# Performance work log

Measured on AMD Instinct MI355X. Metric: run time of the kernel, lower is better.

## Reference

```python
import jax, jax.numpy as jnp
from jax import lax
import numpy as np

B, H, W, C = 8, 64, 64, 128   # NHWC input
F = 256                        # output filters
KH = KW = 3
K = KH * KW
DG = 1                         # deformable groups
CG = C // DG                   # channels per deformable group
PAD_Y, PAD_X = (KH - 1) // 2, (KW - 1) // 2  # SAME padding, stride 1, dilation 1


def setup_inputs() -> dict:
    k1, k2, k3 = jax.random.split(jax.random.key(0), 3)
    return {
        "inputs": jax.random.normal(k1, (B, H, W, C), jnp.float32),
        # conv_offset: Conv2D(dg*3*kh*kw, kernel_size, padding='same', use_bias=True)
        "offset_kernel": jax.random.normal(k2, (KH, KW, C, DG * 3 * K), jnp.float32) * 0.01,
        "offset_bias": jnp.zeros((DG * 3 * K,), jnp.float32),
        # main filter, HWIO as built for channels_last
        "filt": jax.random.normal(k3, (KH, KW, C, F), jnp.float32) * 0.05,
    }


def _deform_conv2d(inputs, offset_kernel, offset_bias, filt):
    # 1) predict offsets + modulation mask with a plain conv (stride 1, SAME)
    wi = lax.conv_general_dilated(
        inputs, offset_kernel, (1, 1), "SAME",
        dimension_numbers=("NHWC", "HWIO", "NHWC")) + offset_bias
    o1, o2, m = jnp.split(wi, 3, axis=-1)           # each [B,H,W,DG*K]
    mask = jax.nn.sigmoid(m).reshape(B, H, W, DG, K)

    # 2) sampling coordinates: base conv grid + learned offsets (o1 = y, o2 = x)
    ky, kx = jnp.meshgrid(jnp.arange(KH), jnp.arange(KW), indexing="ij")
    base_y = (jnp.arange(H)[:, None] - PAD_Y + ky.reshape(-1)[None, :]).astype(jnp.float32)  # [H,K]
    base_x = (jnp.arange(W)[:, None] - PAD_X + kx.reshape(-1)[None, :]).astype(jnp.float32)  # [W,K]
    py = base_y[None, :, None, None, :] + o1.reshape(B, H, W, DG, K)  # [B,H,W,DG,K]
    px = base_x[None, None, :, None, :] + o2.reshape(B, H, W, DG, K)

    # 3) modulated bilinear sampling with zero padding outside the image
    img = inputs.reshape(B, H, W, DG, CG)
    y0f = jnp.floor(py)
    x0f = jnp.floor(px)
    wy1 = py - y0f
    wy0 = 1.0 - wy1
    wx1 = px - x0f
    wx0 = 1.0 - wx1
    bidx = jnp.arange(B)[:, None, None, None, None]
    gidx = jnp.arange(DG)[None, None, None, :, None]

    def corner(yf, xf, wgt):
        valid = (yf >= 0) & (yf <= H - 1) & (xf >= 0) & (xf <= W - 1)
        yi = jnp.clip(yf, 0, H - 1).astype(jnp.int32)
        xi = jnp.clip(xf, 0, W - 1).astype(jnp.int32)
        v = img[bidx, yi, xi, gidx]                  # [B,H,W,DG,K,CG]
        return v * (wgt * valid.astype(jnp.float32))[..., None]

    sampled = (corner(y0f, x0f, wy0 * wx0)
               + corner(y0f, x0f + 1.0, wy0 * wx1)
               + corner(y0f + 1.0, x0f, wy1 * wx0)
               + corner(y0f + 1.0, x0f + 1.0, wy1 * wx1))
    sampled = sampled * mask[..., None]              # DCNv2 modulation

    # 4) im2col columns -> GEMM with the main filter (num_groups = 1)
    cols = jnp.moveaxis(sampled, 3, 4).reshape(B, H, W, K, C)  # channels dg-major
    return jnp.einsum("bhwkc,kcf->bhwf", cols, filt.reshape(K, C, F))


def reference(inputs, offset_kernel, offset_bias, filt):
    return _deform_conv2d(inputs, offset_kernel, offset_bias, filt)
```

## Files before the change

kernel.cpp:

```cpp
#include <hip/hip_runtime.h>
#include <hip/hip_fp16.h>
#include <math.h>

#define B_  8
#define H_  64
#define W_  64
#define C_  128
#define F_  256
#define NOC 27

typedef float    f32x4 __attribute__((ext_vector_type(4)));
typedef _Float16 f16x8 __attribute__((ext_vector_type(8)));

#define FILTT_OFF_F 32768
#define WI32_OFF_F  180224
#define INH_OFF_F   1228800
#define AIM_OFF_F   3325952

static __device__ __forceinline__ unsigned pkh2(float a, float b) {
    __half2 h = __floats2half2_rn(a, b);
    union { __half2 h2; unsigned u; } cv; cv.h2 = h;
    return cv.u;
}

static __device__ __forceinline__ void async16(void* lds, const void* g) {
    __builtin_amdgcn_global_load_lds(
        (const __attribute__((address_space(1))) unsigned int*)g,
        (__attribute__((address_space(3))) unsigned int*)lds, 16, 0, 0);
}

__global__ __launch_bounds__(256) void prep(const float* __restrict__ kofs,
                                            const float* __restrict__ filt,
                                            const float* __restrict__ in,
                                            unsigned short* __restrict__ woffT,
                                            unsigned short* __restrict__ filtT2,
                                            unsigned short* __restrict__ inh) {
    int bidx = blockIdx.x;
    if (bidx >= 1296) {
        int gid = (bidx - 1296) * 256 + threadIdx.x;
        const float4* ip = reinterpret_cast<const float4*>(in) + (size_t)gid * 4;
        float4 a = ip[0], b = ip[1], c = ip[2], d = ip[3];
        uint4 r0 = make_uint4(pkh2(a.x, a.y), pkh2(a.z, a.w), pkh2(b.x, b.y), pkh2(b.z, b.w));
        uint4 r1 = make_uint4(pkh2(c.x, c.y), pkh2(c.z, c.w), pkh2(d.x, d.y), pkh2(d.z, d.w));
        uint4* op = reinterpret_cast<uint4*>(inh) + (size_t)gid * 2;
        op[0] = r0; op[1] = r1;
        return;
    }
    int idx = bidx * 256 + threadIdx.x;
    if (idx < 9 * 32 * 128) {
        int tap = idx >> 12;
        int r   = idx & 4095;
        int oc  = r >> 7;
        int c   = r & 127;
        float v = (oc < NOC) ? kofs[(tap * C_ + c) * NOC + oc] : 0.f;
        union { __half h; unsigned short u; } cv; cv.h = __float2half(v);
        woffT[idx] = cv.u;
        return;
    }
    int idx2 = idx - 9 * 32 * 128;
    if (idx2 < 9 * 256 * 128) {
        int tap = idx2 / 32768;
        int r   = idx2 & 32767;
        int f   = r >> 7;
        int c   = r & 127;
        float v = filt[(tap * C_ + c) * F_ + f];
        union { __half h; unsigned short u; } cv; cv.h = __float2half(v);
        filtT2[(size_t)f * 1152 + tap * 128 + c] = cv.u;
    }
}

__global__ __launch_bounds__(256) void offset_conv_mfma(const unsigned short* __restrict__ inh,
                                                        const unsigned short* __restrict__ woffT,
                                                        const float* __restrict__ bias,
                                                        float* __restrict__ wi32) {
    __shared__ __align__(16) unsigned char win[3 * 66 * 256];

    int t    = threadIdx.x;
    int bid  = blockIdx.x;
    int lg   = ((bid & 7) << 6) | (bid >> 3);
    int bb   = lg >> 6;
    int hh   = lg & 63;
    int pix0 = lg << 6;

    for (int idx = t; idx < 3 * 66 * 16; idx += 256) {
        int ky = idx / (66 * 16);
        int r  = idx % (66 * 16);
        int xi = r >> 4;
        int c8 = r & 15;
        int y  = hh + ky - 1;
        int x  = xi - 1;
        uint4 v = make_uint4(0u, 0u, 0u, 0u);
        if ((unsigned)y < 64u && (unsigned)x < 64u)
            v = *(const uint4*)((const char*)inh +
                    ((size_t)(((bb << 6) + y) * 64 + x) << 8) + (c8 << 4));
        *(uint4*)(win + ky * 16896 + xi * 256 + ((c8 << 4) ^ ((xi & 7) << 4))) = v;
    }
    __syncthreads();

    int lane = t & 63, wv = t >> 6;
    int row  = lane & 15, kg = lane >> 4;
    int px0  = wv << 4;

    f32x4 z = {0.f, 0.f, 0.f, 0.f};
    f32x4 acc[2] = {z, z};

    for (int tap = 0; tap < 9; ++tap) {
        int ky = tap / 3, kx = tap - ky * 3;
        int xi = px0 + row + kx;
        const unsigned char* arow = win + ky * 16896 + xi * 256;
        int sw = (xi & 7) << 4;
        const unsigned short* bp = woffT + (size_t)tap * 4096 + (size_t)row * 128 + kg * 8;
        #pragma unroll
        for (int ks = 0; ks < 4; ++ks) {
            f16x8 a  = *(const f16x8*)(arow + ((ks * 64 + kg * 16) ^ sw));
            f16x8 b0 = *(const f16x8*)(bp + ks * 32);
            f16x8 b1 = *(const f16x8*)(bp + 2048 + ks * 32);
            acc[0] = __builtin_amdgcn_mfma_f32_16x16x32_f16(a, b0, acc[0], 0, 0, 0);
            acc[1] = __builtin_amdgcn_mfma_f32_16x16x32_f16(a, b1, acc[1], 0, 0, 0);
        }
    }

    #pragma unroll
    for (int n = 0; n < 2; ++n) {
        int oc = n * 16 + row;
        float bv = (oc < NOC) ? bias[oc] : 0.f;
        #pragma unroll
        for (int r = 0; r < 4; ++r) {
            int px = px0 + kg * 4 + r;
            wi32[(size_t)(pix0 + px) * 32 + oc] = acc[n][r] + bv;
        }
    }
}

__global__ __launch_bounds__(256) void sample_a(const unsigned short* __restrict__ inh,
                                                const float* __restrict__ wi32,
                                                unsigned short* __restrict__ Aim) {
    __shared__ __align__(16) uint4 offs[8][9];
    __shared__ __align__(16) uint2 wgts[8][9];

    int t   = threadIdx.x;
    int bid = blockIdx.x;
    int lg  = ((bid & 7) << 9) | (bid >> 3);
    int pix0 = lg << 3;

    if (t < 72) {
        int pxl = t / 9, tap = t - pxl * 9;
        int pix = pix0 + pxl;
        int bb  = pix >> 12;
        int hh  = (pix >> 6) & 63;
        int col = pix & 63;
        const float* wp = wi32 + (size_t)pix * 32;
        float o1 = wp[tap], o2 = wp[9 + tap], mm = wp[18 + tap];
        float mask = 1.f / (1.f + __expf(-mm));
        int ky = tap / 3, kx = tap - ky * 3;
        float py  = (float)(hh - 1 + ky) + o1;
        float pxx = (float)(col - 1 + kx) + o2;
        float y0f = floorf(py), x0f = floorf(pxx);
        float wy1 = py - y0f,  wy0 = 1.f - wy1;
        float wx1 = pxx - x0f, wx0 = 1.f - wx1;
        float vy0 = (y0f >=  0.f && y0f <= 63.f) ? 1.f : 0.f;
        float vy1 = (y0f >= -1.f && y0f <= 62.f) ? 1.f : 0.f;
        float vx0 = (x0f >=  0.f && x0f <= 63.f) ? 1.f : 0.f;
        float vx1 = (x0f >= -1.f && x0f <= 62.f) ? 1.f : 0.f;
        int y0 = (int)fminf(fmaxf(y0f,       0.f), 63.f);
        int y1 = (int)fminf(fmaxf(y0f + 1.f, 0.f), 63.f);
        int x0 = (int)fminf(fmaxf(x0f,       0.f), 63.f);
        int x1 = (int)fminf(fmaxf(x0f + 1.f, 0.f), 63.f);
        int base = bb << 12;
        offs[pxl][tap] = make_uint4((unsigned)((base + (y0 << 6) + x0) << 8),
                                    (unsigned)((base + (y0 << 6) + x1) << 8),
                                    (unsigned)((base + (y1 << 6) + x0) << 8),
                                    (unsigned)((base + (y1 << 6) + x1) << 8));
        wgts[pxl][tap] = make_uint2(pkh2(wy0 * wx0 * mask * vy0 * vx0,
                                         wy0 * wx1 * mask * vy0 * vx1),
                                    pkh2(wy1 * wx0 * mask * vy1 * vx0,
                                         wy1 * wx1 * mask * vy1 * vx1));
    }
    __syncthreads();

    int c8  = t & 15;
    int pxl = (t >> 4) & 7;
    int th  = t >> 7;
    int cb  = c8 << 4;

    const char* ih = (const char*)inh;
    char* Ao = (char*)Aim + (size_t)(pix0 + pxl) * 2304;

    int tbeg = th ? 5 : 0, tend = th ? 9 : 5;
    union AU { uint4 u; __half2 h[4]; };
    #pragma unroll 5
    for (int tap = tbeg; tap < tend; ++tap) {
        uint4 O  = offs[pxl][tap];
        uint2 Wp = wgts[pxl][tap];
        union { unsigned u; __half2 h; } w00, w01, w10, w11;
        w00.u = (Wp.x & 0xFFFFu) * 0x10001u;
        w01.u = (Wp.x >> 16)     * 0x10001u;
        w10.u = (Wp.y & 0xFFFFu) * 0x10001u;
        w11.u = (Wp.y >> 16)     * 0x10001u;
        AU c00, c01, c10, c11, s;
        c00.u = *(const uint4*)(ih + O.x + cb);
        c01.u = *(const uint4*)(ih + O.y + cb);
        c10.u = *(const uint4*)(ih + O.z + cb);
        c11.u = *(const uint4*)(ih + O.w + cb);
        #pragma unroll
        for (int j = 0; j < 4; ++j) {
            __half2 sj = __hmul2(c00.h[j], w00.h);
            sj = __hfma2(c01.h[j], w01.h, sj);
            sj = __hfma2(c10.h[j], w10.h, sj);
            s.h[j] = __hfma2(c11.h[j], w11.h, sj);
        }
        *(uint4*)(Ao + tap * 256 + cb) = s.u;
    }
}

__global__ __launch_bounds__(256) void gemm_im2col(const unsigned short* __restrict__ Aim,
                                                   const unsigned short* __restrict__ filtT2,
                                                   float* __restrict__ out) {
    __shared__ __align__(16) unsigned char As[16384];
    __shared__ __align__(16) unsigned char Bs[16384];

    int t   = threadIdx.x;
    int bid = blockIdx.x;
    int lg  = ((bid & 7) << 6) | (bid >> 3);
    int mt  = lg >> 1, nt = lg & 1;
    int apix = mt << 7;
    int f0   = nt << 7;

    int lane = t & 63, wv = t >> 6;
    int wm = wv & 1, wn = wv >> 1;
    int row16 = lane & 15, kg = lane >> 4;

    const char* Ab = (const char*)Aim;
    const char* Bb = (const char*)filtT2;

    f32x4 z = {0.f, 0.f, 0.f, 0.f};
    f32x4 acc[4][4];
    #pragma unroll
    for (int m = 0; m < 4; ++m)
        #pragma unroll
        for (int n = 0; n < 4; ++n) acc[m][n] = z;

    int lin0 = wv * 1024 + lane * 16;

    for (int kb = 0; kb < 18; ++kb) {
        int k2 = kb << 7;
        #pragma unroll
        for (int it = 0; it < 4; ++it) {
            int lin  = lin0 + it * 4096;
            int arow = lin >> 7;
            int acol = (lin & 127) ^ ((arow & 7) << 4);
            async16(As + wv * 1024 + it * 4096,
                    Ab + (size_t)(apix + arow) * 2304 + k2 + acol);
            async16(Bs + wv * 1024 + it * 4096,
                    Bb + (size_t)(f0 + arow) * 2304 + k2 + acol);
        }
        __syncthreads();

        int sw = (row16 & 7) << 4;
        #pragma unroll
        for (int ks = 0; ks < 2; ++ks) {
            int kcol = ((ks << 6) + (kg << 4)) ^ sw;
            f16x8 a[4], b[4];
            #pragma unroll
            for (int m = 0; m < 4; ++m)
                a[m] = *(const f16x8*)(As + ((wm << 6) + (m << 4) + row16) * 128 + kcol);
            #pragma unroll
            for (int n = 0; n < 4; ++n)
                b[n] = *(const f16x8*)(Bs + ((wn << 6) + (n << 4) + row16) * 128 + kcol);
            #pragma unroll
            for (int m = 0; m < 4; ++m)
                #pragma unroll
                for (int n = 0; n < 4; ++n)
                    acc[m][n] = __builtin_amdgcn_mfma_f32_16x16x32_f16(a[m], b[n], acc[m][n], 0, 0, 0);
        }
        __syncthreads();
    }

    int pxb = apix + (wm << 6);
    int fcb = f0 + (wn << 6) + row16;
    #pragma unroll
    for (int m = 0; m < 4; ++m)
        #pragma unroll
        for (int r = 0; r < 4; ++r) {
            int px = pxb + (m << 4) + (kg << 2) + r;
            float* op = out + (size_t)px * 256 + fcb;
            op[0]  = acc[m][0][r];
            op[16] = acc[m][1][r];
            op[32] = acc[m][2][r];
            op[48] = acc[m][3][r];
        }
}

extern "C" void kernel_launch(void* const* d_in, const int* in_sizes, int n_in,
                              void* d_out, int out_size, void* d_ws, size_t ws_size,
                              hipStream_t stream) {
    const float* in   = (const float*)d_in[0];
    const float* kofs = (const float*)d_in[1];
    const float* bias = (const float*)d_in[2];
    const float* filt = (const float*)d_in[3];
    float* out = (float*)d_out;
    float* ws  = (float*)d_ws;

    unsigned short* woffT  = (unsigned short*)ws;
    unsigned short* filtT2 = (unsigned short*)(ws + FILTT_OFF_F);
    float*          wi32   = ws + WI32_OFF_F;
    unsigned short* inh    = (unsigned short*)(ws + INH_OFF_F);
    unsigned short* Aim    = (unsigned short*)(ws + AIM_OFF_F);

    hipLaunchKernelGGL(prep, dim3(2320), dim3(256), 0, stream, kofs, filt, in, woffT, filtT2, inh);
    hipLaunchKernelGGL(offset_conv_mfma, dim3(512), dim3(256), 0, stream, inh, woffT, bias, wi32);
    hipLaunchKernelGGL(sample_a, dim3(4096), dim3(256), 0, stream, inh, wi32, Aim);
    hipLaunchKernelGGL(gemm_im2col, dim3(512), dim3(256), 0, stream, Aim, filtT2, out);
}
```

Baseline: 76.78 us.

## Fuse bilinear sampling into im2col GEMM with double-buffered LDS pipeline

Removes the separate sample_a kernel and the materialized fp16 im2col buffer. The GEMM kernel now computes the bilinear sampling parameters per pixel and tap, gathers the four corners and blends them directly into swizzled LDS A tiles. Two ping-pong A/B buffers overlap the next tap's gathers and async filter loads with the current MFMA work. This saves one launch and the Aim write and read, but the sampling work is repeated for each of the two N tiles and register pressure rises.

```diff
diff --git a/kernel.cpp b/kernel.cpp
--- a/kernel.cpp
+++ b/kernel.cpp
@@ -15,7 +15,6 @@
 #define FILTT_OFF_F 32768
 #define WI32_OFF_F  180224
 #define INH_OFF_F   1228800
-#define AIM_OFF_F   3325952
 
 static __device__ __forceinline__ unsigned pkh2(float a, float b) {
     __half2 h = __floats2half2_rn(a, b);
@@ -132,92 +131,101 @@
     }
 }
 
-__global__ __launch_bounds__(256) void sample_a(const unsigned short* __restrict__ inh,
-                                                const float* __restrict__ wi32,
-                                                unsigned short* __restrict__ Aim) {
-    __shared__ __align__(16) uint4 offs[8][9];
-    __shared__ __align__(16) uint2 wgts[8][9];
-
-    int t   = threadIdx.x;
-    int bid = blockIdx.x;
-    int lg  = ((bid & 7) << 9) | (bid >> 3);
-    int pix0 = lg << 3;
-
-    if (t < 72) {
-        int pxl = t / 9, tap = t - pxl * 9;
-        int pix = pix0 + pxl;
-        int bb  = pix >> 12;
-        int hh  = (pix >> 6) & 63;
-        int col = pix & 63;
-        const float* wp = wi32 + (size_t)pix * 32;
-        float o1 = wp[tap], o2 = wp[9 + tap], mm = wp[18 + tap];
-        float mask = 1.f / (1.f + __expf(-mm));
-        int ky = tap / 3, kx = tap - ky * 3;
-        float py  = (float)(hh - 1 + ky) + o1;
-        float pxx = (float)(col - 1 + kx) + o2;
-        float y0f = floorf(py), x0f = floorf(pxx);
-        float wy1 = py - y0f,  wy0 = 1.f - wy1;
-        float wx1 = pxx - x0f, wx0 = 1.f - wx1;
-        float vy0 = (y0f >=  0.f && y0f <= 63.f) ? 1.f : 0.f;
-        float vy1 = (y0f >= -1.f && y0f <= 62.f) ? 1.f : 0.f;
-        float vx0 = (x0f >=  0.f && x0f <= 63.f) ? 1.f : 0.f;
-        float vx1 = (x0f >= -1.f && x0f <= 62.f) ? 1.f : 0.f;
-        int y0 = (int)fminf(fmaxf(y0f,       0.f), 63.f);
-        int y1 = (int)fminf(fmaxf(y0f + 1.f, 0.f), 63.f);
-        int x0 = (int)fminf(fmaxf(x0f,       0.f), 63.f);
-        int x1 = (int)fminf(fmaxf(x0f + 1.f, 0.f), 63.f);
-        int base = bb << 12;
-        offs[pxl][tap] = make_uint4((unsigned)((base + (y0 << 6) + x0) << 8),
-                                    (unsigned)((base + (y0 << 6) + x1) << 8),
-                                    (unsigned)((base + (y1 << 6) + x0) << 8),
-                                    (unsigned)((base + (y1 << 6) + x1) << 8));
-        wgts[pxl][tap] = make_uint2(pkh2(wy0 * wx0 * mask * vy0 * vx0,
-                                         wy0 * wx1 * mask * vy0 * vx1),
-                                    pkh2(wy1 * wx0 * mask * vy1 * vx0,
-                                         wy1 * wx1 * mask * vy1 * vx1));
-    }
-    __syncthreads();
-
-    int c8  = t & 15;
-    int pxl = (t >> 4) & 7;
-    int th  = t >> 7;
-    int cb  = c8 << 4;
-
-    const char* ih = (const char*)inh;
-    char* Ao = (char*)Aim + (size_t)(pix0 + pxl) * 2304;
-
-    int tbeg = th ? 5 : 0, tend = th ? 9 : 5;
-    union AU { uint4 u; __half2 h[4]; };
-    #pragma unroll 5
-    for (int tap = tbeg; tap < tend; ++tap) {
-        uint4 O  = offs[pxl][tap];
-        uint2 Wp = wgts[pxl][tap];
-        union { unsigned u; __half2 h; } w00, w01, w10, w11;
-        w00.u = (Wp.x & 0xFFFFu) * 0x10001u;
-        w01.u = (Wp.x >> 16)     * 0x10001u;
-        w10.u = (Wp.y & 0xFFFFu) * 0x10001u;
-        w11.u = (Wp.y >> 16)     * 0x10001u;
-        AU c00, c01, c10, c11, s;
-        c00.u = *(const uint4*)(ih + O.x + cb);
-        c01.u = *(const uint4*)(ih + O.y + cb);
-        c10.u = *(const uint4*)(ih + O.z + cb);
-        c11.u = *(const uint4*)(ih + O.w + cb);
-        #pragma unroll
-        for (int j = 0; j < 4; ++j) {
-            __half2 sj = __hmul2(c00.h[j], w00.h);
-            sj = __hfma2(c01.h[j], w01.h, sj);
-            sj = __hfma2(c10.h[j], w10.h, sj);
-            s.h[j] = __hfma2(c11.h[j], w11.h, sj);
-        }
-        *(uint4*)(Ao + tap * 256 + cb) = s.u;
-    }
-}
-
-__global__ __launch_bounds__(256) void gemm_im2col(const unsigned short* __restrict__ Aim,
-                                                   const unsigned short* __restrict__ filtT2,
-                                                   float* __restrict__ out) {
-    __shared__ __align__(16) unsigned char As[16384];
-    __shared__ __align__(16) unsigned char Bs[16384];
+struct Par { unsigned o00, o01, o10, o11, wa, wb; };
+
+static __device__ __forceinline__ Par mkpar(float o1, float o2, float mm,
+                                            int hh, int col, int bb, int tap) {
+    float mask = 1.f / (1.f + __expf(-mm));
+    int ky = tap / 3, kx = tap - ky * 3;
+    float py  = (float)(hh - 1 + ky) + o1;
+    float pxx = (float)(col - 1 + kx) + o2;
+    float y0f = floorf(py), x0f = floorf(pxx);
+    float wy1 = py - y0f,  wy0 = 1.f - wy1;
+    float wx1 = pxx - x0f, wx0 = 1.f - wx1;
+    float vy0 = (y0f >=  0.f && y0f <= 63.f) ? 1.f : 0.f;
+    float vy1 = (y0f >= -1.f && y0f <= 62.f) ? 1.f : 0.f;
+    float vx0 = (x0f >=  0.f && x0f <= 63.f) ? 1.f : 0.f;
+    float vx1 = (x0f >= -1.f && x0f <= 62.f) ? 1.f : 0.f;
+    int y0 = (int)fminf(fmaxf(y0f,       0.f), 63.f);
+    int y1 = (int)fminf(fmaxf(y0f + 1.f, 0.f), 63.f);
+    int x0 = (int)fminf(fmaxf(x0f,       0.f), 63.f);
+    int x1 = (int)fminf(fmaxf(x0f + 1.f, 0.f), 63.f);
+    int base = bb << 12;
+    Par p;
+    p.o00 = (unsigned)((base + (y0 << 6) + x0) << 8);
+    p.o01 = (unsigned)((base + (y0 << 6) + x1) << 8);
+    p.o10 = (unsigned)((base + (y1 << 6) + x0) << 8);
+    p.o11 = (unsigned)((base + (y1 << 6) + x1) << 8);
+    p.wa  = pkh2(wy0 * wx0 * mask * vy0 * vx0, wy0 * wx1 * mask * vy0 * vx1);
+    p.wb  = pkh2(wy1 * wx0 * mask * vy1 * vx0, wy1 * wx1 * mask * vy1 * vx1);
+    return p;
+}
+
+static __device__ __forceinline__ void issue_corners(uint4 cc[4][4], const char* ih,
+                                                     const Par& p, int chb) {
+    #pragma unroll
+    for (int j = 0; j < 4; ++j) cc[0][j] = *(const uint4*)(ih + p.o00 + chb + j * 16);
+    #pragma unroll
+    for (int j = 0; j < 4; ++j) cc[1][j] = *(const uint4*)(ih + p.o01 + chb + j * 16);
+    #pragma unroll
+    for (int j = 0; j < 4; ++j) cc[2][j] = *(const uint4*)(ih + p.o10 + chb + j * 16);
+    #pragma unroll
+    for (int j = 0; j < 4; ++j) cc[3][j] = *(const uint4*)(ih + p.o11 + chb + j * 16);
+}
+
+static __device__ __forceinline__ void blend_write(unsigned char* dst, int spx, int cp,
+                                                   const uint4 cc[4][4],
+                                                   unsigned wa, unsigned wb) {
+    union H2 { unsigned u; __half2 h; };
+    H2 w00, w01, w10, w11;
+    w00.u = (wa & 0xFFFFu) * 0x10001u;
+    w01.u = (wa >> 16)     * 0x10001u;
+    w10.u = (wb & 0xFFFFu) * 0x10001u;
+    w11.u = (wb >> 16)     * 0x10001u;
+    #pragma unroll
+    for (int j = 0; j < 4; ++j) {
+        union { uint4 u; __half2 h[4]; } a0, a1, a2, a3, s;
+        a0.u = cc[0][j]; a1.u = cc[1][j]; a2.u = cc[2][j]; a3.u = cc[3][j];
+        #pragma unroll
+        for (int q = 0; q < 4; ++q) {
+            __half2 v = __hmul2(a0.h[q], w00.h);
+            v = __hfma2(a1.h[q], w01.h, v);
+            v = __hfma2(a2.h[q], w10.h, v);
+            s.h[q] = __hfma2(a3.h[q], w11.h, v);
+        }
+        int c8 = cp * 4 + j;
+        *(uint4*)(dst + spx * 128 + ((c8 * 16) ^ ((spx & 7) << 4))) = s.u;
+    }
+}
+
+static __device__ __forceinline__ void do_mfma(const unsigned char* As, const unsigned char* Bs,
+                                               int wm, int wn, int row16, int kg,
+                                               f32x4 acc[4][4]) {
+    int sw = (row16 & 7) << 4;
+    #pragma unroll
+    for (int ks = 0; ks < 2; ++ks) {
+        int kcol = ((ks << 6) + (kg << 4)) ^ sw;
+        f16x8 a[4], b[4];
+        #pragma unroll
+        for (int m = 0; m < 4; ++m)
+            a[m] = *(const f16x8*)(As + ((wm << 6) + (m << 4) + row16) * 128 + kcol);
+        #pragma unroll
+        for (int n = 0; n < 4; ++n)
+            b[n] = *(const f16x8*)(Bs + ((wn << 6) + (n << 4) + row16) * 128 + kcol);
+        #pragma unroll
+        for (int m = 0; m < 4; ++m)
+            #pragma unroll
+            for (int n = 0; n < 4; ++n)
+                acc[m][n] = __builtin_amdgcn_mfma_f32_16x16x32_f16(a[m], b[n], acc[m][n], 0, 0, 0);
+    }
+}
+
+__global__ __launch_bounds__(256, 2) void gemm_fused(const unsigned short* __restrict__ inh,
+                                                     const unsigned short* __restrict__ filtT2,
+                                                     const float* __restrict__ wi32,
+                                                     float* __restrict__ out) {
+    __shared__ __align__(16) unsigned char As0[16384], As1[16384];
+    __shared__ __align__(16) unsigned char Bs0[16384], Bs1[16384];
 
     int t   = threadIdx.x;
     int bid = blockIdx.x;
@@ -226,13 +234,20 @@
     int apix = mt << 7;
     int f0   = nt << 7;
 
+    int spx = t & 127;
+    int cp  = t >> 7;
+    int pix = apix + spx;
+    int bb  = pix >> 12, hh = (pix >> 6) & 63, col = pix & 63;
+    const float* wrow = wi32 + (size_t)pix * 32;
+    const char*  ih   = (const char*)inh;
+
     int lane = t & 63, wv = t >> 6;
+    int lin0 = wv * 1024 + lane * 16;
+    const char* Bb = (const char*)filtT2;
+
     int wm = wv & 1, wn = wv >> 1;
     int row16 = lane & 15, kg = lane >> 4;
 
-    const char* Ab = (const char*)Aim;
-    const char* Bb = (const char*)filtT2;
-
     f32x4 z = {0.f, 0.f, 0.f, 0.f};
     f32x4 acc[4][4];
     #pragma unroll
@@ -240,39 +255,50 @@
         #pragma unroll
         for (int n = 0; n < 4; ++n) acc[m][n] = z;
 
-    int lin0 = wv * 1024 + lane * 16;
-
-    for (int kb = 0; kb < 18; ++kb) {
-        int k2 = kb << 7;
+    uint4 cc[4][4];
+    Par par;
+    float no1, no2, nmm;
+
+    auto asyncB = [&](unsigned char* buf, int s) {
         #pragma unroll
         for (int it = 0; it < 4; ++it) {
             int lin  = lin0 + it * 4096;
-            int arow = lin >> 7;
-            int acol = (lin & 127) ^ ((arow & 7) << 4);
-            async16(As + wv * 1024 + it * 4096,
-                    Ab + (size_t)(apix + arow) * 2304 + k2 + acol);
-            async16(Bs + wv * 1024 + it * 4096,
-                    Bb + (size_t)(f0 + arow) * 2304 + k2 + acol);
-        }
+            int brow = lin >> 7;
+            int bcol = (lin & 127) ^ ((brow & 7) << 4);
+            async16(buf + wv * 1024 + it * 4096,
+                    Bb + (size_t)(f0 + brow) * 2304 + s * 128 + bcol);
+        }
+    };
+
+    {
+        float o1 = wrow[0], o2 = wrow[9], mm = wrow[18];
+        par = mkpar(o1, o2, mm, hh, col, bb, 0);
+        issue_corners(cc, ih, par, cp * 64);
+        asyncB(Bs0, 0);
+        no1 = wrow[1]; no2 = wrow[10]; nmm = wrow[19];
+        blend_write(As0, spx, cp, cc, par.wa, par.wb);
         __syncthreads();
-
-        int sw = (row16 & 7) << 4;
-        #pragma unroll
-        for (int ks = 0; ks < 2; ++ks) {
-            int kcol = ((ks << 6) + (kg << 4)) ^ sw;
-            f16x8 a[4], b[4];
-            #pragma unroll
-            for (int m = 0; m < 4; ++m)
-                a[m] = *(const f16x8*)(As + ((wm << 6) + (m << 4) + row16) * 128 + kcol);
-            #pragma unroll
-            for (int n = 0; n < 4; ++n)
-                b[n] = *(const f16x8*)(Bs + ((wn << 6) + (n << 4) + row16) * 128 + kcol);
-            #pragma unroll
-            for (int m = 0; m < 4; ++m)
-                #pragma unroll
-                for (int n = 0; n < 4; ++n)
-                    acc[m][n] = __builtin_amdgcn_mfma_f32_16x16x32_f16(a[m], b[n], acc[m][n], 0, 0, 0);
-        }
+    }
+
+    for (int tap = 0; tap < 9; ++tap) {
+        issue_corners(cc, ih, par, 128 + cp * 64);
+        asyncB(Bs1, 2 * tap + 1);
+        __builtin_amdgcn_sched_barrier(0);
+        do_mfma(As0, Bs0, wm, wn, row16, kg, acc);
+        blend_write(As1, spx, cp, cc, par.wa, par.wb);
+        __syncthreads();
+
+        if (tap < 8) {
+            par = mkpar(no1, no2, nmm, hh, col, bb, tap + 1);
+            if (tap < 7) {
+                no1 = wrow[tap + 2]; no2 = wrow[11 + tap]; nmm = wrow[20 + tap];
+            }
+            issue_corners(cc, ih, par, cp * 64);
+            asyncB(Bs0, 2 * tap + 2);
+            __builtin_amdgcn_sched_barrier(0);
+        }
+        do_mfma(As1, Bs1, wm, wn, row16, kg, acc);
+        if (tap < 8) blend_write(As0, spx, cp, cc, par.wa, par.wb);
         __syncthreads();
     }
 
@@ -305,10 +331,8 @@
     unsigned short* filtT2 = (unsigned short*)(ws + FILTT_OFF_F);
     float*          wi32   = ws + WI32_OFF_F;
     unsigned short* inh    = (unsigned short*)(ws + INH_OFF_F);
-    unsigned short* Aim    = (unsigned short*)(ws + AIM_OFF_F);
 
     hipLaunchKernelGGL(prep, dim3(2320), dim3(256), 0, stream, kofs, filt, in, woffT, filtT2, inh);
     hipLaunchKernelGGL(offset_conv_mfma, dim3(512), dim3(256), 0, stream, inh, woffT, bias, wi32);
-    hipLaunchKernelGGL(sample_a, dim3(4096), dim3(256), 0, stream, inh, wi32, Aim);
-    hipLaunchKernelGGL(gemm_im2col, dim3(512), dim3(256), 0, stream, Aim, filtT2, out);
-}
+    hipLaunchKernelGGL(gemm_fused, dim3(512), dim3(256), 0, stream, inh, filtT2, wi32, out);
+}
```

Measured after the change: 114.3 us. 1.49x slower.

## Fuse offset conv with bilinear sampling and double-buffer GEMM LDS stages

Applied to the files above, without the earlier changes.

Merges the offset-prediction conv and the bilinear sampling kernel into one per-row kernel, so offsets and mask stay in shared memory and are never written to or reread from a global buffer. This also removes one kernel launch. Separately, the im2col GEMM now double-buffers its A/B LDS tiles so the async loads for the next K-step are issued before the MFMAs on the current one. The fused kernel runs only 512 blocks, where the old sampling kernel used 4096, and both kernels use more LDS, which can lower occupancy and hurt latency hiding in the gather loop.

```diff
diff --git a/kernel.cpp b/kernel.cpp
--- a/kernel.cpp
+++ b/kernel.cpp
@@ -13,7 +13,6 @@
 typedef _Float16 f16x8 __attribute__((ext_vector_type(8)));
 
 #define FILTT_OFF_F 32768
-#define WI32_OFF_F  180224
 #define INH_OFF_F   1228800
 #define AIM_OFF_F   3325952
 
@@ -69,11 +68,14 @@
     }
 }
 
-__global__ __launch_bounds__(256) void offset_conv_mfma(const unsigned short* __restrict__ inh,
-                                                        const unsigned short* __restrict__ woffT,
-                                                        const float* __restrict__ bias,
-                                                        float* __restrict__ wi32) {
+__global__ __launch_bounds__(256) void sample_row(const unsigned short* __restrict__ inh,
+                                                  const unsigned short* __restrict__ woffT,
+                                                  const float* __restrict__ bias,
+                                                  unsigned short* __restrict__ Aim) {
     __shared__ __align__(16) unsigned char win[3 * 66 * 256];
+    __shared__ float wi[64][33];
+    __shared__ __align__(16) uint4 prmo[64][9];
+    __shared__ __align__(16) uint2 prmw[64][9];
 
     int t    = threadIdx.x;
     int bid  = blockIdx.x;
@@ -97,64 +99,48 @@
     }
     __syncthreads();
 
-    int lane = t & 63, wv = t >> 6;
-    int row  = lane & 15, kg = lane >> 4;
-    int px0  = wv << 4;
-
-    f32x4 z = {0.f, 0.f, 0.f, 0.f};
-    f32x4 acc[2] = {z, z};
-
-    for (int tap = 0; tap < 9; ++tap) {
-        int ky = tap / 3, kx = tap - ky * 3;
-        int xi = px0 + row + kx;
-        const unsigned char* arow = win + ky * 16896 + xi * 256;
-        int sw = (xi & 7) << 4;
-        const unsigned short* bp = woffT + (size_t)tap * 4096 + (size_t)row * 128 + kg * 8;
-        #pragma unroll
-        for (int ks = 0; ks < 4; ++ks) {
-            f16x8 a  = *(const f16x8*)(arow + ((ks * 64 + kg * 16) ^ sw));
-            f16x8 b0 = *(const f16x8*)(bp + ks * 32);
-            f16x8 b1 = *(const f16x8*)(bp + 2048 + ks * 32);
-            acc[0] = __builtin_amdgcn_mfma_f32_16x16x32_f16(a, b0, acc[0], 0, 0, 0);
-            acc[1] = __builtin_amdgcn_mfma_f32_16x16x32_f16(a, b1, acc[1], 0, 0, 0);
-        }
-    }
-
-    #pragma unroll
-    for (int n = 0; n < 2; ++n) {
-        int oc = n * 16 + row;
-        float bv = (oc < NOC) ? bias[oc] : 0.f;
-        #pragma unroll
-        for (int r = 0; r < 4; ++r) {
-            int px = px0 + kg * 4 + r;
-            wi32[(size_t)(pix0 + px) * 32 + oc] = acc[n][r] + bv;
-        }
-    }
-}
-
-__global__ __launch_bounds__(256) void sample_a(const unsigned short* __restrict__ inh,
-                                                const float* __restrict__ wi32,
-                                                unsigned short* __restrict__ Aim) {
-    __shared__ __align__(16) uint4 offs[8][9];
-    __shared__ __align__(16) uint2 wgts[8][9];
-
-    int t   = threadIdx.x;
-    int bid = blockIdx.x;
-    int lg  = ((bid & 7) << 9) | (bid >> 3);
-    int pix0 = lg << 3;
-
-    if (t < 72) {
-        int pxl = t / 9, tap = t - pxl * 9;
-        int pix = pix0 + pxl;
-        int bb  = pix >> 12;
-        int hh  = (pix >> 6) & 63;
-        int col = pix & 63;
-        const float* wp = wi32 + (size_t)pix * 32;
-        float o1 = wp[tap], o2 = wp[9 + tap], mm = wp[18 + tap];
+    {
+        int lane = t & 63, wv = t >> 6;
+        int row  = lane & 15, kg = lane >> 4;
+        int px0  = wv << 4;
+
+        f32x4 z = {0.f, 0.f, 0.f, 0.f};
+        f32x4 acc[2] = {z, z};
+
+        for (int tap = 0; tap < 9; ++tap) {
+            int ky = tap / 3, kx = tap - ky * 3;
+            int xi = px0 + row + kx;
+            const unsigned char* arow = win + ky * 16896 + xi * 256;
+            int sw = (xi & 7) << 4;
+            const unsigned short* bp = woffT + (size_t)tap * 4096 + (size_t)row * 128 + kg * 8;
+            #pragma unroll
+            for (int ks = 0; ks < 4; ++ks) {
+                f16x8 a  = *(const f16x8*)(arow + ((ks * 64 + kg * 16) ^ sw));
+                f16x8 b0 = *(const f16x8*)(bp + ks * 32);
+                f16x8 b1 = *(const f16x8*)(bp + 2048 + ks * 32);
+                acc[0] = __builtin_amdgcn_mfma_f32_16x16x32_f16(a, b0, acc[0], 0, 0, 0);
+                acc[1] = __builtin_amdgcn_mfma_f32_16x16x32_f16(a, b1, acc[1], 0, 0, 0);
+            }
+        }
+        #pragma unroll
+        for (int n = 0; n < 2; ++n) {
+            int oc = n * 16 + row;
+            float bv = (oc < NOC) ? bias[oc] : 0.f;
+            #pragma unroll
+            for (int r = 0; r < 4; ++r)
+                wi[px0 + kg * 4 + r][oc] = acc[n][r] + bv;
+        }
+    }
+    __syncthreads();
+
+    for (int it = t; it < 576; it += 256) {
+        int px  = it & 63;
+        int tap = it >> 6;
+        float o1 = wi[px][tap], o2 = wi[px][9 + tap], mm = wi[px][18 + tap];
         float mask = 1.f / (1.f + __expf(-mm));
         int ky = tap / 3, kx = tap - ky * 3;
         float py  = (float)(hh - 1 + ky) + o1;
-        float pxx = (float)(col - 1 + kx) + o2;
+        float pxx = (float)(px - 1 + kx) + o2;
         float y0f = floorf(py), x0f = floorf(pxx);
         float wy1 = py - y0f,  wy0 = 1.f - wy1;
         float wx1 = pxx - x0f, wx0 = 1.f - wx1;
@@ -167,57 +153,61 @@
         int x0 = (int)fminf(fmaxf(x0f,       0.f), 63.f);
         int x1 = (int)fminf(fmaxf(x0f + 1.f, 0.f), 63.f);
         int base = bb << 12;
-        offs[pxl][tap] = make_uint4((unsigned)((base + (y0 << 6) + x0) << 8),
-                                    (unsigned)((base + (y0 << 6) + x1) << 8),
-                                    (unsigned)((base + (y1 << 6) + x0) << 8),
-                                    (unsigned)((base + (y1 << 6) + x1) << 8));
-        wgts[pxl][tap] = make_uint2(pkh2(wy0 * wx0 * mask * vy0 * vx0,
-                                         wy0 * wx1 * mask * vy0 * vx1),
-                                    pkh2(wy1 * wx0 * mask * vy1 * vx0,
-                                         wy1 * wx1 * mask * vy1 * vx1));
+        prmo[px][tap] = make_uint4((unsigned)((base + (y0 << 6) + x0) << 8),
+                                   (unsigned)((base + (y0 << 6) + x1) << 8),
+                                   (unsigned)((base + (y1 << 6) + x0) << 8),
+                                   (unsigned)((base + (y1 << 6) + x1) << 8));
+        prmw[px][tap] = make_uint2(pkh2(wy0 * wx0 * mask * vy0 * vx0,
+                                        wy0 * wx1 * mask * vy0 * vx1),
+                                   pkh2(wy1 * wx0 * mask * vy1 * vx0,
+                                        wy1 * wx1 * mask * vy1 * vx1));
     }
     __syncthreads();
 
     int c8  = t & 15;
-    int pxl = (t >> 4) & 7;
+    int pxg = (t >> 4) & 7;
     int th  = t >> 7;
     int cb  = c8 << 4;
 
     const char* ih = (const char*)inh;
-    char* Ao = (char*)Aim + (size_t)(pix0 + pxl) * 2304;
-
     int tbeg = th ? 5 : 0, tend = th ? 9 : 5;
     union AU { uint4 u; __half2 h[4]; };
-    #pragma unroll 5
-    for (int tap = tbeg; tap < tend; ++tap) {
-        uint4 O  = offs[pxl][tap];
-        uint2 Wp = wgts[pxl][tap];
-        union { unsigned u; __half2 h; } w00, w01, w10, w11;
-        w00.u = (Wp.x & 0xFFFFu) * 0x10001u;
-        w01.u = (Wp.x >> 16)     * 0x10001u;
-        w10.u = (Wp.y & 0xFFFFu) * 0x10001u;
-        w11.u = (Wp.y >> 16)     * 0x10001u;
-        AU c00, c01, c10, c11, s;
-        c00.u = *(const uint4*)(ih + O.x + cb);
-        c01.u = *(const uint4*)(ih + O.y + cb);
-        c10.u = *(const uint4*)(ih + O.z + cb);
-        c11.u = *(const uint4*)(ih + O.w + cb);
-        #pragma unroll
-        for (int j = 0; j < 4; ++j) {
-            __half2 sj = __hmul2(c00.h[j], w00.h);
-            sj = __hfma2(c01.h[j], w01.h, sj);
-            sj = __hfma2(c10.h[j], w10.h, sj);
-            s.h[j] = __hfma2(c11.h[j], w11.h, sj);
-        }
-        *(uint4*)(Ao + tap * 256 + cb) = s.u;
+
+    #pragma unroll 2
+    for (int pp = 0; pp < 8; ++pp) {
+        int px = pxg + (pp << 3);
+        char* Ao = (char*)Aim + (size_t)(pix0 + px) * 2304;
+        #pragma unroll 5
+        for (int tap = tbeg; tap < tend; ++tap) {
+            uint4 O  = prmo[px][tap];
+            uint2 Wp = prmw[px][tap];
+            union { unsigned u; __half2 h; } w00, w01, w10, w11;
+            w00.u = (Wp.x & 0xFFFFu) * 0x10001u;
+            w01.u = (Wp.x >> 16)     * 0x10001u;
+            w10.u = (Wp.y & 0xFFFFu) * 0x10001u;
+            w11.u = (Wp.y >> 16)     * 0x10001u;
+            AU c00, c01, c10, c11, s;
+            c00.u = *(const uint4*)(ih + O.x + cb);
+            c01.u = *(const uint4*)(ih + O.y + cb);
+            c10.u = *(const uint4*)(ih + O.z + cb);
+            c11.u = *(const uint4*)(ih + O.w + cb);
+            #pragma unroll
+            for (int j = 0; j < 4; ++j) {
+                __half2 sj = __hmul2(c00.h[j], w00.h);
+                sj = __hfma2(c01.h[j], w01.h, sj);
+                sj = __hfma2(c10.h[j], w10.h, sj);
+                s.h[j] = __hfma2(c11.h[j], w11.h, sj);
+            }
+            *(uint4*)(Ao + tap * 256 + cb) = s.u;
+        }
     }
 }
 
 __global__ __launch_bounds__(256) void gemm_im2col(const unsigned short* __restrict__ Aim,
                                                    const unsigned short* __restrict__ filtT2,
                                                    float* __restrict__ out) {
-    __shared__ __align__(16) unsigned char As[16384];
-    __shared__ __align__(16) unsigned char Bs[16384];
+    __shared__ __align__(16) unsigned char As[2][16384];
+    __shared__ __align__(16) unsigned char Bs[2][16384];
 
     int t   = threadIdx.x;
     int bid = blockIdx.x;
@@ -242,20 +232,21 @@
 
     int lin0 = wv * 1024 + lane * 16;
 
-    for (int kb = 0; kb < 18; ++kb) {
-        int k2 = kb << 7;
+    auto stageTo = [&](unsigned char* A, unsigned char* B, int s) {
+        int k2 = s << 7;
         #pragma unroll
         for (int it = 0; it < 4; ++it) {
-            int lin  = lin0 + it * 4096;
-            int arow = lin >> 7;
-            int acol = (lin & 127) ^ ((arow & 7) << 4);
-            async16(As + wv * 1024 + it * 4096,
-                    Ab + (size_t)(apix + arow) * 2304 + k2 + acol);
-            async16(Bs + wv * 1024 + it * 4096,
-                    Bb + (size_t)(f0 + arow) * 2304 + k2 + acol);
-        }
-        __syncthreads();
-
+            int lin = lin0 + it * 4096;
+            int r_  = lin >> 7;
+            int c_  = (lin & 127) ^ ((r_ & 7) << 4);
+            async16(A + wv * 1024 + it * 4096,
+                    Ab + (size_t)(apix + r_) * 2304 + k2 + c_);
+            async16(B + wv * 1024 + it * 4096,
+                    Bb + (size_t)(f0 + r_) * 2304 + k2 + c_);
+        }
+    };
+
+    auto mfmaOn = [&](const unsigned char* A, const unsigned char* B) {
         int sw = (row16 & 7) << 4;
         #pragma unroll
         for (int ks = 0; ks < 2; ++ks) {
@@ -263,16 +254,28 @@
             f16x8 a[4], b[4];
             #pragma unroll
             for (int m = 0; m < 4; ++m)
-                a[m] = *(const f16x8*)(As + ((wm << 6) + (m << 4) + row16) * 128 + kcol);
+                a[m] = *(const f16x8*)(A + ((wm << 6) + (m << 4) + row16) * 128 + kcol);
             #pragma unroll
             for (int n = 0; n < 4; ++n)
-                b[n] = *(const f16x8*)(Bs + ((wn << 6) + (n << 4) + row16) * 128 + kcol);
+                b[n] = *(const f16x8*)(B + ((wn << 6) + (n << 4) + row16) * 128 + kcol);
             #pragma unroll
             for (int m = 0; m < 4; ++m)
                 #pragma unroll
                 for (int n = 0; n < 4; ++n)
                     acc[m][n] = __builtin_amdgcn_mfma_f32_16x16x32_f16(a[m], b[n], acc[m][n], 0, 0, 0);
         }
+    };
+
+    stageTo(As[0], Bs[0], 0);
+    __syncthreads();
+
+    #pragma unroll 1
+    for (int kb = 0; kb < 18; kb += 2) {
+        stageTo(As[1], Bs[1], kb + 1);
+        mfmaOn(As[0], Bs[0]);
+        __syncthreads();
+        if (kb < 16) stageTo(As[0], Bs[0], kb + 2);
+        mfmaOn(As[1], Bs[1]);
         __syncthreads();
     }
 
@@ -303,12 +306,10 @@
 
     unsigned short* woffT  = (unsigned short*)ws;
     unsigned short* filtT2 = (unsigned short*)(ws + FILTT_OFF_F);
-    float*          wi32   = ws + WI32_OFF_F;
     unsigned short* inh    = (unsigned short*)(ws + INH_OFF_F);
     unsigned short* Aim    = (unsigned short*)(ws + AIM_OFF_F);
 
     hipLaunchKernelGGL(prep, dim3(2320), dim3(256), 0, stream, kofs, filt, in, woffT, filtT2, inh);
-    hipLaunchKernelGGL(offset_conv_mfma, dim3(512), dim3(256), 0, stream, inh, woffT, bias, wi32);
-    hipLaunchKernelGGL(sample_a, dim3(4096), dim3(256), 0, stream, inh, wi32, Aim);
+    hipLaunchKernelGGL(sample_row, dim3(512), dim3(256), 0, stream, inh, woffT, bias, Aim);
     hipLaunchKernelGGL(gemm_im2col, dim3(512), dim3(256), 0, stream, Aim, filtT2, out);
 }
```

After: 73.41 us, median of 2. -4.4%, faster.

## Fuse bilinear sampling and im2col GEMM with producer/consumer warp specialization

Applied to the files above, without the earlier changes.

Merges the sampling kernel and the im2col GEMM into one kernel, so the fp16 im2col matrix is no longer written to and re-read from global memory. Within each 512-thread block, four waves gather and modulate the samples for one tap into a double-buffered LDS ring. The other four waves run MFMA on that tap, reading filter fragments directly from global memory and raising their priority with s_setprio. Each block now covers a 64-pixel row across all 256 filters. In exchange, filter loads are no longer staged through LDS, and the gather and compute stages are serialized by a block barrier on every tap.

```diff
diff --git a/kernel.cpp b/kernel.cpp
--- a/kernel.cpp
+++ b/kernel.cpp
@@ -15,18 +15,11 @@
 #define FILTT_OFF_F 32768
 #define WI32_OFF_F  180224
 #define INH_OFF_F   1228800
-#define AIM_OFF_F   3325952
 
 static __device__ __forceinline__ unsigned pkh2(float a, float b) {
     __half2 h = __floats2half2_rn(a, b);
     union { __half2 h2; unsigned u; } cv; cv.h2 = h;
     return cv.u;
-}
-
-static __device__ __forceinline__ void async16(void* lds, const void* g) {
-    __builtin_amdgcn_global_load_lds(
-        (const __attribute__((address_space(1))) unsigned int*)g,
-        (__attribute__((address_space(3))) unsigned int*)lds, 16, 0, 0);
 }
 
 __global__ __launch_bounds__(256) void prep(const float* __restrict__ kofs,
@@ -132,29 +125,33 @@
     }
 }
 
-__global__ __launch_bounds__(256) void sample_a(const unsigned short* __restrict__ inh,
-                                                const float* __restrict__ wi32,
-                                                unsigned short* __restrict__ Aim) {
-    __shared__ __align__(16) uint4 offs[8][9];
-    __shared__ __align__(16) uint2 wgts[8][9];
-
-    int t   = threadIdx.x;
-    int bid = blockIdx.x;
-    int lg  = ((bid & 7) << 9) | (bid >> 3);
-    int pix0 = lg << 3;
-
-    if (t < 72) {
-        int pxl = t / 9, tap = t - pxl * 9;
-        int pix = pix0 + pxl;
-        int bb  = pix >> 12;
-        int hh  = (pix >> 6) & 63;
-        int col = pix & 63;
-        const float* wp = wi32 + (size_t)pix * 32;
+__global__ __launch_bounds__(512, 4) void dcn_fused(const unsigned short* __restrict__ inh,
+                                                    const unsigned short* __restrict__ filtT2,
+                                                    const float* __restrict__ wi32,
+                                                    float* __restrict__ out) {
+    __shared__ __align__(16) unsigned char ring[2][64 * 256];
+    __shared__ __align__(16) uint4 prmo[64][9];
+    __shared__ __align__(16) uint2 prmw[64][9];
+
+    int t    = threadIdx.x;
+    int bid  = blockIdx.x;
+    int lg   = ((bid & 7) << 6) | (bid >> 3);
+    int bb   = lg >> 6;
+    int hh   = lg & 63;
+    int pix0 = lg << 6;
+
+    const char* ih = (const char*)inh;
+    const char* Bb = (const char*)filtT2;
+
+    for (int it = t; it < 576; it += 512) {
+        int px  = it & 63;
+        int tap = it >> 6;
+        const float* wp = wi32 + (size_t)(pix0 + px) * 32;
         float o1 = wp[tap], o2 = wp[9 + tap], mm = wp[18 + tap];
         float mask = 1.f / (1.f + __expf(-mm));
         int ky = tap / 3, kx = tap - ky * 3;
         float py  = (float)(hh - 1 + ky) + o1;
-        float pxx = (float)(col - 1 + kx) + o2;
+        float pxx = (float)(px - 1 + kx) + o2;
         float y0f = floorf(py), x0f = floorf(pxx);
         float wy1 = py - y0f,  wy0 = 1.f - wy1;
         float wx1 = pxx - x0f, wx0 = 1.f - wx1;
@@ -167,128 +164,108 @@
         int x0 = (int)fminf(fmaxf(x0f,       0.f), 63.f);
         int x1 = (int)fminf(fmaxf(x0f + 1.f, 0.f), 63.f);
         int base = bb << 12;
-        offs[pxl][tap] = make_uint4((unsigned)((base + (y0 << 6) + x0) << 8),
-                                    (unsigned)((base + (y0 << 6) + x1) << 8),
-                                    (unsigned)((base + (y1 << 6) + x0) << 8),
-                                    (unsigned)((base + (y1 << 6) + x1) << 8));
-        wgts[pxl][tap] = make_uint2(pkh2(wy0 * wx0 * mask * vy0 * vx0,
-                                         wy0 * wx1 * mask * vy0 * vx1),
-                                    pkh2(wy1 * wx0 * mask * vy1 * vx0,
-                                         wy1 * wx1 * mask * vy1 * vx1));
+        prmo[px][tap] = make_uint4((unsigned)((base + (y0 << 6) + x0) << 8),
+                                   (unsigned)((base + (y0 << 6) + x1) << 8),
+                                   (unsigned)((base + (y1 << 6) + x0) << 8),
+                                   (unsigned)((base + (y1 << 6) + x1) << 8));
+        prmw[px][tap] = make_uint2(pkh2(wy0 * wx0 * mask * vy0 * vx0,
+                                        wy0 * wx1 * mask * vy0 * vx1),
+                                   pkh2(wy1 * wx0 * mask * vy1 * vx0,
+                                        wy1 * wx1 * mask * vy1 * vx1));
     }
     __syncthreads();
 
-    int c8  = t & 15;
-    int pxl = (t >> 4) & 7;
-    int th  = t >> 7;
-    int cb  = c8 << 4;
-
-    const char* ih = (const char*)inh;
-    char* Ao = (char*)Aim + (size_t)(pix0 + pxl) * 2304;
-
-    int tbeg = th ? 5 : 0, tend = th ? 9 : 5;
+    int lane  = t & 63;
+    int wv    = t >> 6;
+    bool cons = (wv < 4);
+    int row16 = lane & 15, kg = lane >> 4;
+    const char* fb = Bb + (size_t)((wv << 6) + row16) * 2304 + (kg << 4);
+    int sw = (row16 & 7) << 4;
+    int pl = t & 255;
+    int ppx = pl >> 2;
+    int pq  = pl & 3;
+
+    f32x4 z = {0.f, 0.f, 0.f, 0.f};
+    f32x4 acc[4][4];
+    #pragma unroll
+    for (int m = 0; m < 4; ++m)
+        #pragma unroll
+        for (int n = 0; n < 4; ++n) acc[m][n] = z;
+
     union AU { uint4 u; __half2 h[4]; };
-    #pragma unroll 5
-    for (int tap = tbeg; tap < tend; ++tap) {
-        uint4 O  = offs[pxl][tap];
-        uint2 Wp = wgts[pxl][tap];
+
+    auto gather = [&](int tap, int slot) {
+        uint4 O  = prmo[ppx][tap];
+        uint2 Wp = prmw[ppx][tap];
         union { unsigned u; __half2 h; } w00, w01, w10, w11;
         w00.u = (Wp.x & 0xFFFFu) * 0x10001u;
         w01.u = (Wp.x >> 16)     * 0x10001u;
         w10.u = (Wp.y & 0xFFFFu) * 0x10001u;
         w11.u = (Wp.y >> 16)     * 0x10001u;
-        AU c00, c01, c10, c11, s;
-        c00.u = *(const uint4*)(ih + O.x + cb);
-        c01.u = *(const uint4*)(ih + O.y + cb);
-        c10.u = *(const uint4*)(ih + O.z + cb);
-        c11.u = *(const uint4*)(ih + O.w + cb);
         #pragma unroll
         for (int j = 0; j < 4; ++j) {
-            __half2 sj = __hmul2(c00.h[j], w00.h);
-            sj = __hfma2(c01.h[j], w01.h, sj);
-            sj = __hfma2(c10.h[j], w10.h, sj);
-            s.h[j] = __hfma2(c11.h[j], w11.h, sj);
-        }
-        *(uint4*)(Ao + tap * 256 + cb) = s.u;
-    }
-}
-
-__global__ __launch_bounds__(256) void gemm_im2col(const unsigned short* __restrict__ Aim,
-                                                   const unsigned short* __restrict__ filtT2,
-                                                   float* __restrict__ out) {
-    __shared__ __align__(16) unsigned char As[16384];
-    __shared__ __align__(16) unsigned char Bs[16384];
-
-    int t   = threadIdx.x;
-    int bid = blockIdx.x;
-    int lg  = ((bid & 7) << 6) | (bid >> 3);
-    int mt  = lg >> 1, nt = lg & 1;
-    int apix = mt << 7;
-    int f0   = nt << 7;
-
-    int lane = t & 63, wv = t >> 6;
-    int wm = wv & 1, wn = wv >> 1;
-    int row16 = lane & 15, kg = lane >> 4;
-
-    const char* Ab = (const char*)Aim;
-    const char* Bb = (const char*)filtT2;
-
-    f32x4 z = {0.f, 0.f, 0.f, 0.f};
-    f32x4 acc[4][4];
-    #pragma unroll
-    for (int m = 0; m < 4; ++m)
-        #pragma unroll
-        for (int n = 0; n < 4; ++n) acc[m][n] = z;
-
-    int lin0 = wv * 1024 + lane * 16;
-
-    for (int kb = 0; kb < 18; ++kb) {
-        int k2 = kb << 7;
-        #pragma unroll
-        for (int it = 0; it < 4; ++it) {
-            int lin  = lin0 + it * 4096;
-            int arow = lin >> 7;
-            int acol = (lin & 127) ^ ((arow & 7) << 4);
-            async16(As + wv * 1024 + it * 4096,
-                    Ab + (size_t)(apix + arow) * 2304 + k2 + acol);
-            async16(Bs + wv * 1024 + it * 4096,
-                    Bb + (size_t)(f0 + arow) * 2304 + k2 + acol);
-        }
-        __syncthreads();
-
-        int sw = (row16 & 7) << 4;
-        #pragma unroll
-        for (int ks = 0; ks < 2; ++ks) {
-            int kcol = ((ks << 6) + (kg << 4)) ^ sw;
-            f16x8 a[4], b[4];
+            int cbj = (pq << 6) + (j << 4);
+            AU c00, c01, c10, c11, s;
+            c00.u = *(const uint4*)(ih + O.x + cbj);
+            c01.u = *(const uint4*)(ih + O.y + cbj);
+            c10.u = *(const uint4*)(ih + O.z + cbj);
+            c11.u = *(const uint4*)(ih + O.w + cbj);
             #pragma unroll
-            for (int m = 0; m < 4; ++m)
-                a[m] = *(const f16x8*)(As + ((wm << 6) + (m << 4) + row16) * 128 + kcol);
+            for (int q = 0; q < 4; ++q) {
+                __half2 sj = __hmul2(c00.h[q], w00.h);
+                sj = __hfma2(c01.h[q], w01.h, sj);
+                sj = __hfma2(c10.h[q], w10.h, sj);
+                s.h[q] = __hfma2(c11.h[q], w11.h, sj);
+            }
+            *(uint4*)(ring[slot] + (ppx << 8) + (cbj ^ ((ppx & 7) << 4))) = s.u;
+        }
+    };
+
+    if (!cons) gather(0, 0);
+    __syncthreads();
+
+    #pragma unroll 1
+    for (int tap = 0; tap < 9; ++tap) {
+        if (cons) {
+            const unsigned char* A = ring[tap & 1];
+            const char* ft = fb + (size_t)tap * 256;
+            __builtin_amdgcn_s_setprio(1);
             #pragma unroll
-            for (int n = 0; n < 4; ++n)
-                b[n] = *(const f16x8*)(Bs + ((wn << 6) + (n << 4) + row16) * 128 + kcol);
-            #pragma unroll
-            for (int m = 0; m < 4; ++m)
+            for (int ks = 0; ks < 4; ++ks) {
+                int kcol = ((ks << 6) + (kg << 4)) ^ sw;
+                f16x8 a[4], b[4];
+                #pragma unroll
+                for (int m = 0; m < 4; ++m)
+                    a[m] = *(const f16x8*)(A + ((m * 16 + row16) << 8) + kcol);
                 #pragma unroll
                 for (int n = 0; n < 4; ++n)
-                    acc[m][n] = __builtin_amdgcn_mfma_f32_16x16x32_f16(a[m], b[n], acc[m][n], 0, 0, 0);
+                    b[n] = *(const f16x8*)(ft + (size_t)n * 16 * 2304 + (ks << 6));
+                #pragma unroll
+                for (int m = 0; m < 4; ++m)
+                    #pragma unroll
+                    for (int n = 0; n < 4; ++n)
+                        acc[m][n] = __builtin_amdgcn_mfma_f32_16x16x32_f16(a[m], b[n], acc[m][n], 0, 0, 0);
+            }
+            __builtin_amdgcn_s_setprio(0);
+        } else {
+            if (tap < 8) gather(tap + 1, (tap + 1) & 1);
         }
         __syncthreads();
     }
 
-    int pxb = apix + (wm << 6);
-    int fcb = f0 + (wn << 6) + row16;
-    #pragma unroll
-    for (int m = 0; m < 4; ++m)
-        #pragma unroll
-        for (int r = 0; r < 4; ++r) {
-            int px = pxb + (m << 4) + (kg << 2) + r;
-            float* op = out + (size_t)px * 256 + fcb;
-            op[0]  = acc[m][0][r];
-            op[16] = acc[m][1][r];
-            op[32] = acc[m][2][r];
-            op[48] = acc[m][3][r];
-        }
+    if (cons) {
+        #pragma unroll
+        for (int m = 0; m < 4; ++m)
+            #pragma unroll
+            for (int r = 0; r < 4; ++r) {
+                int px = m * 16 + (kg << 2) + r;
+                float* op = out + (size_t)(pix0 + px) * 256 + (wv << 6) + row16;
+                op[0]  = acc[m][0][r];
+                op[16] = acc[m][1][r];
+                op[32] = acc[m][2][r];
+                op[48] = acc[m][3][r];
+            }
+    }
 }
 
 extern "C" void kernel_launch(void* const* d_in, const int* in_sizes, int n_in,
@@ -305,10 +282,8 @@
     unsigned short* filtT2 = (unsigned short*)(ws + FILTT_OFF_F);
     float*          wi32   = ws + WI32_OFF_F;
     unsigned short* inh    = (unsigned short*)(ws + INH_OFF_F);
-    unsigned short* Aim    = (unsigned short*)(ws + AIM_OFF_F);
 
     hipLaunchKernelGGL(prep, dim3(2320), dim3(256), 0, stream, kofs, filt, in, woffT, filtT2, inh);
     hipLaunchKernelGGL(offset_conv_mfma, dim3(512), dim3(256), 0, stream, inh, woffT, bias, wi32);
-    hipLaunchKernelGGL(sample_a, dim3(4096), dim3(256), 0, stream, inh, wi32, Aim);
-    hipLaunchKernelGGL(gemm_im2col, dim3(512), dim3(256), 0, stream, Aim, filtT2, out);
-}
+    hipLaunchKernelGGL(dcn_fused, dim3(512), dim3(512), 0, stream, inh, filtT2, wi32, out);
+}
```

Result: slower. 106.3 us (+38.5%).
